# Optimization experiments

Hardware: AMD Instinct MI355X
Metric: run time of the kernel (lower is better)

The kernel has to match this reference:

```python
import jax, jax.numpy as jnp
import numpy as np

N_PROJ, N_SP, D, H = 400000, 40000, 256, 8
DH = D // H  # 32
EPS = 1e-5
NEG_SLOPE = 0.2  # GATv2Conv default


def layer_norm(x, g, b):
    m = x.mean(-1, keepdims=True)
    v = ((x - m) ** 2).mean(-1, keepdims=True)
    return (x - m) / jnp.sqrt(v + EPS) * g + b


def setup_inputs() -> dict:
    key = jax.random.key(0)
    ks = jax.random.split(key, 8)
    w = lambda k, shape: jax.random.normal(k, shape, jnp.float32) * 0.05
    return dict(
        proj_features=jax.random.normal(ks[0], (N_PROJ, D), jnp.float32),
        prev_scenepoint_features=jax.random.normal(ks[1], (N_SP, D), jnp.float32),
        Wl=w(ks[2], (D, D)), bl=jnp.zeros((D,), jnp.float32),
        Wr=w(ks[3], (D, D)), br=jnp.zeros((D,), jnp.float32),
        att=w(ks[4], (H, DH)), gat_bias=jnp.zeros((D,), jnp.float32),
        ln1_g=jnp.ones((D,), jnp.float32), ln1_b=jnp.zeros((D,), jnp.float32),
        ln2_g=jnp.ones((D,), jnp.float32), ln2_b=jnp.zeros((D,), jnp.float32),
        mlp_W=w(ks[5], (D, D)), mlp_b=jnp.zeros((D,), jnp.float32),
        edge_src=jnp.arange(N_PROJ, dtype=jnp.int32),
        edge_tgt=jax.random.randint(ks[6], (N_PROJ,), 0, N_SP, jnp.int32),
    )


def reference(proj_features, prev_scenepoint_features, Wl, bl, Wr, br, att,
              gat_bias, ln1_g, ln1_b, ln2_g, ln2_b, mlp_W, mlp_b,
              edge_src, edge_tgt):
    # norm_and_proj_scenepoint2proj: LayerNorm + ReLU (no Linear: dims equal)
    x_agg = jax.nn.relu(layer_norm(prev_scenepoint_features, ln1_g, ln1_b))

    # GATv2Conv: lin_l on source (projection) nodes, lin_r on target (scene point) nodes
    xl = (proj_features @ Wl + bl).reshape(N_PROJ, H, DH)   # [Np,H,DH]
    xr = (x_agg @ Wr + br).reshape(N_SP, H, DH)             # [Ns,H,DH]
    xl_e = xl[edge_src]                                     # [E,H,DH]
    xr_e = xr[edge_tgt]                                     # [E,H,DH]
    e = jnp.einsum('ehd,hd->eh', jax.nn.leaky_relu(xl_e + xr_e, NEG_SLOPE), att)

    # segment softmax over edges sharing the same target scene point
    e_max = jax.ops.segment_max(e, edge_tgt, num_segments=N_SP)
    ex = jnp.exp(e - e_max[edge_tgt])
    denom = jax.ops.segment_sum(ex, edge_tgt, num_segments=N_SP)
    alpha = ex / (denom[edge_tgt] + 1e-16)                  # [E,H]

    out = jax.ops.segment_sum(alpha[..., None] * xl_e, edge_tgt, num_segments=N_SP)
    x = out.reshape(N_SP, D) + gat_bias                     # concat heads + bias

    # stateful residual with previous scene point features
    x = prev_scenepoint_features + x
    x_skip = x
    # norm_pre_mlp + ReLU, then mlp (single Linear since n_hidden_layers=0)
    x = jax.nn.relu(layer_norm(x, ln2_g, ln2_b))
    x = x @ mlp_W + mlp_b
    return x_skip + x
```

## Files before the change

### kernel.cpp

```cpp
#include <hip/hip_runtime.h>
#include <hip/hip_bf16.h>

#define D_DIM 256
#define EPS_LN 1e-5f
#define NEG_SLOPE 0.2f

typedef __bf16 bf16x8 __attribute__((ext_vector_type(8)));
typedef unsigned short ushortx8 __attribute__((ext_vector_type(8)));
typedef unsigned short ushortx4 __attribute__((ext_vector_type(4)));
typedef float floatx4 __attribute__((ext_vector_type(4)));

__device__ inline unsigned short f2bf(float f) {
    __hip_bfloat16 h = __float2bfloat16(f);
    return __builtin_bit_cast(unsigned short, h);
}
__device__ inline float bf2f(unsigned short u) {
    unsigned int x = ((unsigned int)u) << 16;
    return __builtin_bit_cast(float, x);
}

__global__ __launch_bounds__(256) void wtrans_kernel(
        const float* __restrict__ W0, const float* __restrict__ W1,
        const float* __restrict__ W2, unsigned short* __restrict__ T0,
        unsigned short* __restrict__ T1, unsigned short* __restrict__ T2) {
    const float* W = (blockIdx.y == 0) ? W0 : (blockIdx.y == 1) ? W1 : W2;
    unsigned short* T = (blockIdx.y == 0) ? T0 : (blockIdx.y == 1) ? T1 : T2;
    __shared__ float lds[64][65];
    const int tx = blockIdx.x & 3;
    const int ty = blockIdx.x >> 2;
    const int t = threadIdx.x;
    const int r = t >> 6;
    const int c = t & 63;
#pragma unroll
    for (int i = 0; i < 16; ++i) {
        int row = ty * 64 + r + i * 4;
        lds[r + i * 4][c] = W[row * 256 + tx * 64 + c];
    }
    __syncthreads();
#pragma unroll
    for (int i = 0; i < 16; ++i) {
        int orow = tx * 64 + r + i * 4;
        T[orow * 256 + ty * 64 + c] = f2bf(lds[c][r + i * 4]);
    }
}

__global__ __launch_bounds__(256) void ln_relu_kernel(
        const float* __restrict__ x, const float* __restrict__ g,
        const float* __restrict__ b, float* __restrict__ y, int nrows) {
    int row = blockIdx.x * 4 + (threadIdx.x >> 6);
    if (row >= nrows) return;
    int lane = threadIdx.x & 63;
    float4 v = ((const float4*)(x + (size_t)row * D_DIM))[lane];
    float s = v.x + v.y + v.z + v.w;
    float s2 = v.x * v.x + v.y * v.y + v.z * v.z + v.w * v.w;
#pragma unroll
    for (int m = 32; m >= 1; m >>= 1) {
        s += __shfl_xor(s, m, 64);
        s2 += __shfl_xor(s2, m, 64);
    }
    float mean = s * (1.f / D_DIM);
    float var = s2 * (1.f / D_DIM) - mean * mean;
    float rstd = rsqrtf(var + EPS_LN);
    float4 gv = ((const float4*)g)[lane];
    float4 bv = ((const float4*)b)[lane];
    float4 o;
    o.x = fmaxf((v.x - mean) * rstd * gv.x + bv.x, 0.f);
    o.y = fmaxf((v.y - mean) * rstd * gv.y + bv.y, 0.f);
    o.z = fmaxf((v.z - mean) * rstd * gv.z + bv.z, 0.f);
    o.w = fmaxf((v.w - mean) * rstd * gv.w + bv.w, 0.f);
    ((float4*)(y + (size_t)row * D_DIM))[lane] = o;
}

template <int OUT_BF16, int HAS_RES>
__global__ __launch_bounds__(256) void gemm256_kernel(
        const float* __restrict__ A, const unsigned short* __restrict__ Wt,
        const float* __restrict__ bias, const float* __restrict__ res,
        void* __restrict__ out, int M) {
    __shared__ unsigned short As[2][128 * 40];
    __shared__ unsigned short Bs[2][128 * 40];
    const int n0 = blockIdx.x * 128;
    const int m0 = blockIdx.y * 128;
    const int t = threadIdx.x;
    const int lane = t & 63;
    const int wave = t >> 6;
    const int q = lane >> 4;
    const int l16 = lane & 15;
    const int wm = (wave & 1) * 64;
    const int wn = (wave >> 1) * 64;
    const int sm = t >> 1;
    const int sh = t & 1;

    const bool arow_ok = (m0 + sm) < M;
    const float* aptr = A + (size_t)(m0 + sm) * 256 + sh * 16;
    const unsigned short* bptr = Wt + (size_t)(n0 + sm) * 256 + sh * 16;

    float4 a_reg[4];
    ushortx8 b_reg[2];

    auto g_load = [&](int kt) {
        if (arow_ok) {
            const float4* ap = (const float4*)(aptr + kt * 32);
            a_reg[0] = ap[0]; a_reg[1] = ap[1]; a_reg[2] = ap[2]; a_reg[3] = ap[3];
        }
        const ushortx8* bp = (const ushortx8*)(bptr + kt * 32);
        b_reg[0] = bp[0]; b_reg[1] = bp[1];
    };
    auto s_store = [&](int buf) {
        unsigned short tmp[16];
        if (arow_ok) {
#pragma unroll
            for (int i = 0; i < 4; ++i) {
                tmp[i * 4 + 0] = f2bf(a_reg[i].x);
                tmp[i * 4 + 1] = f2bf(a_reg[i].y);
                tmp[i * 4 + 2] = f2bf(a_reg[i].z);
                tmp[i * 4 + 3] = f2bf(a_reg[i].w);
            }
        } else {
#pragma unroll
            for (int i = 0; i < 16; ++i) tmp[i] = 0;
        }
        *(ushortx8*)&As[buf][sm * 40 + sh * 16] = *(ushortx8*)&tmp[0];
        *(ushortx8*)&As[buf][sm * 40 + sh * 16 + 8] = *(ushortx8*)&tmp[8];
        *(ushortx8*)&Bs[buf][sm * 40 + sh * 16] = b_reg[0];
        *(ushortx8*)&Bs[buf][sm * 40 + sh * 16 + 8] = b_reg[1];
    };

    floatx4 acc[4][4] = {};

    g_load(0);
    s_store(0);
    __syncthreads();

    for (int kt = 0; kt < 8; ++kt) {
        const int cur = kt & 1;
        if (kt < 7) g_load(kt + 1);
        bf16x8 af[4], bfr[4];
#pragma unroll
        for (int mi = 0; mi < 4; ++mi)
            af[mi] = __builtin_bit_cast(bf16x8,
                *(const ushortx8*)&As[cur][(wm + mi * 16 + l16) * 40 + q * 8]);
#pragma unroll
        for (int ni = 0; ni < 4; ++ni)
            bfr[ni] = __builtin_bit_cast(bf16x8,
                *(const ushortx8*)&Bs[cur][(wn + ni * 16 + l16) * 40 + q * 8]);
#pragma unroll
        for (int mi = 0; mi < 4; ++mi)
#pragma unroll
            for (int ni = 0; ni < 4; ++ni)
                acc[mi][ni] = __builtin_amdgcn_mfma_f32_16x16x32_bf16(
                    af[mi], bfr[ni], acc[mi][ni], 0, 0, 0);
        if (kt < 7) {
            s_store(cur ^ 1);
            __syncthreads();
        }
    }

#pragma unroll
    for (int mi = 0; mi < 4; ++mi) {
#pragma unroll
        for (int ni = 0; ni < 4; ++ni) {
            int col = n0 + wn + ni * 16 + l16;
            float bcol = bias[col];
#pragma unroll
            for (int r = 0; r < 4; ++r) {
                int row = m0 + wm + mi * 16 + q * 4 + r;
                if (row < M) {
                    float v = acc[mi][ni][r] + bcol;
                    if (HAS_RES) v += res[(size_t)row * 256 + col];
                    if (OUT_BF16)
                        ((unsigned short*)out)[(size_t)row * 256 + col] = f2bf(v);
                    else
                        ((float*)out)[(size_t)row * 256 + col] = v;
                }
            }
        }
    }
}

__global__ void hist_kernel(const int* __restrict__ tgt, int* __restrict__ counts, int E) {
    int i = blockIdx.x * 256 + threadIdx.x;
    if (i < E) atomicAdd(&counts[tgt[i]], 1);
}

__global__ __launch_bounds__(1024) void scan_kernel(
        const int* __restrict__ counts, int* __restrict__ offs, int n) {
    __shared__ int lds[1024];
    int t = threadIdx.x;
    int CH = (n + 1023) >> 10;
    int beg = t * CH, end = min(beg + CH, n);
    int s = 0;
    for (int i = beg; i < end; ++i) s += counts[i];
    lds[t] = s;
    __syncthreads();
    for (int off = 1; off < 1024; off <<= 1) {
        int v = (t >= off) ? lds[t - off] : 0;
        __syncthreads();
        lds[t] += v;
        __syncthreads();
    }
    int run = lds[t] - s;
    for (int i = beg; i < end; ++i) { offs[i] = run; run += counts[i]; }
    if (t == 1023) offs[n] = lds[1023];
}

__global__ void scatter_kernel(const int* __restrict__ tgt, const int* __restrict__ offs,
                               int* __restrict__ cursor, int* __restrict__ elist, int E) {
    int i = blockIdx.x * 256 + threadIdx.x;
    if (i < E) {
        int tg = tgt[i];
        int p = atomicAdd(&cursor[tg], 1);
        elist[offs[tg] + p] = i;
    }
}

__global__ __launch_bounds__(256) void aggregate_kernel(
        const unsigned short* __restrict__ xl, const float* __restrict__ xr,
        const float* __restrict__ prev, const int* __restrict__ esrc,
        const int* __restrict__ elist, const int* __restrict__ offs,
        const float* __restrict__ att, const float* __restrict__ gbias,
        const float* __restrict__ g2, const float* __restrict__ b2,
        float* __restrict__ x_skip, float* __restrict__ h2, int nsp) {
    int tgt = blockIdx.x * 4 + (threadIdx.x >> 6);
    if (tgt >= nsp) return;
    int lane = threadIdx.x & 63;
    float4 xrv = ((const float4*)(xr + (size_t)tgt * D_DIM))[lane];
    float4 attv = ((const float4*)att)[lane];
    float acc0 = 0.f, acc1 = 0.f, acc2 = 0.f, acc3 = 0.f, den = 0.f;
    int beg = offs[tgt], end = offs[tgt + 1];

    ushortx4 row = {};
    if (beg < end) {
        int e = elist[beg];
        int src = esrc[e];
        row = ((const ushortx4*)(xl + (size_t)src * D_DIM))[lane];
    }
    for (int i = beg; i < end; ++i) {
        ushortx4 row_n = {};
        if (i + 1 < end) {
            int e1 = elist[i + 1];
            int s1 = esrc[e1];
            row_n = ((const ushortx4*)(xl + (size_t)s1 * D_DIM))[lane];
        }
        float x0 = bf2f(row[0]), x1 = bf2f(row[1]), x2 = bf2f(row[2]), x3 = bf2f(row[3]);
        float t0 = x0 + xrv.x, t1 = x1 + xrv.y, t2 = x2 + xrv.z, t3 = x3 + xrv.w;
        t0 = t0 > 0.f ? t0 : NEG_SLOPE * t0;
        t1 = t1 > 0.f ? t1 : NEG_SLOPE * t1;
        t2 = t2 > 0.f ? t2 : NEG_SLOPE * t2;
        t3 = t3 > 0.f ? t3 : NEG_SLOPE * t3;
        float p = t0 * attv.x + t1 * attv.y + t2 * attv.z + t3 * attv.w;
        p += __shfl_xor(p, 1, 64);
        p += __shfl_xor(p, 2, 64);
        p += __shfl_xor(p, 4, 64);
        float ex = __expf(p);
        den += ex;
        acc0 += ex * x0; acc1 += ex * x1; acc2 += ex * x2; acc3 += ex * x3;
        row = row_n;
    }
    float rden = 1.f / (den + 1e-16f);
    float4 pv = ((const float4*)(prev + (size_t)tgt * D_DIM))[lane];
    float4 gb = ((const float4*)gbias)[lane];
    float v0 = pv.x + acc0 * rden + gb.x;
    float v1 = pv.y + acc1 * rden + gb.y;
    float v2 = pv.z + acc2 * rden + gb.z;
    float v3 = pv.w + acc3 * rden + gb.w;
    float s = v0 + v1 + v2 + v3;
    float s2 = v0 * v0 + v1 * v1 + v2 * v2 + v3 * v3;
#pragma unroll
    for (int m = 32; m >= 1; m >>= 1) {
        s += __shfl_xor(s, m, 64);
        s2 += __shfl_xor(s2, m, 64);
    }
    float mean = s * (1.f / D_DIM);
    float var = s2 * (1.f / D_DIM) - mean * mean;
    float rstd = rsqrtf(var + EPS_LN);
    float4 g2v = ((const float4*)g2)[lane];
    float4 b2v = ((const float4*)b2)[lane];
    float4 xs; xs.x = v0; xs.y = v1; xs.z = v2; xs.w = v3;
    ((float4*)(x_skip + (size_t)tgt * D_DIM))[lane] = xs;
    float4 h;
    h.x = fmaxf((v0 - mean) * rstd * g2v.x + b2v.x, 0.f);
    h.y = fmaxf((v1 - mean) * rstd * g2v.y + b2v.y, 0.f);
    h.z = fmaxf((v2 - mean) * rstd * g2v.z + b2v.z, 0.f);
    h.w = fmaxf((v3 - mean) * rstd * g2v.w + b2v.w, 0.f);
    ((float4*)(h2 + (size_t)tgt * D_DIM))[lane] = h;
}

extern "C" void kernel_launch(void* const* d_in, const int* in_sizes, int n_in,
                              void* d_out, int out_size, void* d_ws, size_t ws_size,
                              hipStream_t stream) {
    const float* proj = (const float*)d_in[0];
    const float* prev = (const float*)d_in[1];
    const float* Wl   = (const float*)d_in[2];
    const float* bl   = (const float*)d_in[3];
    const float* Wr   = (const float*)d_in[4];
    const float* br   = (const float*)d_in[5];
    const float* att  = (const float*)d_in[6];
    const float* gbias= (const float*)d_in[7];
    const float* ln1g = (const float*)d_in[8];
    const float* ln1b = (const float*)d_in[9];
    const float* ln2g = (const float*)d_in[10];
    const float* ln2b = (const float*)d_in[11];
    const float* Wm   = (const float*)d_in[12];
    const float* mb   = (const float*)d_in[13];
    const int* esrc   = (const int*)d_in[14];
    const int* etgt   = (const int*)d_in[15];

    const int NP = in_sizes[0] / D_DIM;
    const int NS = in_sizes[1] / D_DIM;
    const int E  = in_sizes[14];

    char* base = (char*)d_ws;
    size_t off = 0;
    auto carve = [&](size_t bytes) {
        char* p = base + off;
        off += (bytes + 255) & ~(size_t)255;
        return p;
    };
    unsigned short* xl    = (unsigned short*)carve((size_t)NP * D_DIM * 2);
    float* x_agg          = (float*)carve((size_t)NS * D_DIM * 4);
    float* xr             = (float*)carve((size_t)NS * D_DIM * 4);
    float* x_skip         = (float*)carve((size_t)NS * D_DIM * 4);
    float* h2             = (float*)carve((size_t)NS * D_DIM * 4);
    unsigned short* Wt_l  = (unsigned short*)carve((size_t)D_DIM * D_DIM * 2);
    unsigned short* Wt_r  = (unsigned short*)carve((size_t)D_DIM * D_DIM * 2);
    unsigned short* Wt_m  = (unsigned short*)carve((size_t)D_DIM * D_DIM * 2);
    int* counts           = (int*)carve((size_t)NS * 4 * 2);
    int* cursor           = counts + NS;
    int* offs             = (int*)carve((size_t)(NS + 1) * 4);
    int* elist            = (int*)carve((size_t)E * 4);

    hipMemsetAsync(counts, 0, (size_t)NS * 4 * 2, stream);

    wtrans_kernel<<<dim3(16, 3), 256, 0, stream>>>(Wl, Wr, Wm, Wt_l, Wt_r, Wt_m);

    ln_relu_kernel<<<(NS + 3) / 4, 256, 0, stream>>>(prev, ln1g, ln1b, x_agg, NS);

    gemm256_kernel<0, 0><<<dim3(2, (NS + 127) / 128), 256, 0, stream>>>(
        x_agg, Wt_r, br, nullptr, (void*)xr, NS);

    gemm256_kernel<1, 0><<<dim3(2, (NP + 127) / 128), 256, 0, stream>>>(
        proj, Wt_l, bl, nullptr, (void*)xl, NP);

    hist_kernel<<<(E + 255) / 256, 256, 0, stream>>>(etgt, counts, E);
    scan_kernel<<<1, 1024, 0, stream>>>(counts, offs, NS);
    scatter_kernel<<<(E + 255) / 256, 256, 0, stream>>>(etgt, offs, cursor, elist, E);

    aggregate_kernel<<<(NS + 3) / 4, 256, 0, stream>>>(
        xl, xr, prev, esrc, elist, offs, att, gbias, ln2g, ln2b, x_skip, h2, NS);

    gemm256_kernel<0, 1><<<dim3(2, (NS + 127) / 128), 256, 0, stream>>>(
        h2, Wt_m, mb, x_skip, d_out, NS);
}
```

Baseline: 1.048 ms.

## Stage GEMM tiles via async global-to-LDS copies and store source ids in edge list

The GEMM now loads fp32 A tiles and bf16 weight tiles straight from global memory into LDS with global_load_lds, using XOR-swizzled layouts. The fp32-to-bf16 conversion moves to fragment-read time, and launch bounds request 3 blocks per SM. This drops the register staging round-trip and overlaps the next tile's loads with MFMA work, but it doubles A's LDS footprint and repeats the conversion for each wave. Separately, the scatter kernel writes source ids directly, so the aggregate kernel skips one dependent indirection per edge.

```diff
diff --git a/kernel.cpp b/kernel.cpp
--- a/kernel.cpp
+++ b/kernel.cpp
@@ -17,6 +17,19 @@
 __device__ inline float bf2f(unsigned short u) {
     unsigned int x = ((unsigned int)u) << 16;
     return __builtin_bit_cast(float, x);
+}
+
+__device__ __forceinline__ void async_copy16(const void* g, void* l) {
+    __builtin_amdgcn_global_load_lds(
+        (const __attribute__((address_space(1))) unsigned int*)g,
+        (__attribute__((address_space(3))) unsigned int*)l, 16, 0, 0);
+}
+
+__device__ inline bf16x8 cvt_frag(float4 a, float4 b) {
+    ushortx8 u;
+    u[0] = f2bf(a.x); u[1] = f2bf(a.y); u[2] = f2bf(a.z); u[3] = f2bf(a.w);
+    u[4] = f2bf(b.x); u[5] = f2bf(b.y); u[6] = f2bf(b.z); u[7] = f2bf(b.w);
+    return __builtin_bit_cast(bf16x8, u);
 }
 
 __global__ __launch_bounds__(256) void wtrans_kernel(
@@ -72,12 +85,12 @@
 }
 
 template <int OUT_BF16, int HAS_RES>
-__global__ __launch_bounds__(256) void gemm256_kernel(
+__global__ __launch_bounds__(256, 3) void gemm256_kernel(
         const float* __restrict__ A, const unsigned short* __restrict__ Wt,
         const float* __restrict__ bias, const float* __restrict__ res,
         void* __restrict__ out, int M) {
-    __shared__ unsigned short As[2][128 * 40];
-    __shared__ unsigned short Bs[2][128 * 40];
+    __shared__ float As[2][128 * 32];
+    __shared__ unsigned short Bs[2][128 * 32];
     const int n0 = blockIdx.x * 128;
     const int m0 = blockIdx.y * 128;
     const int t = threadIdx.x;
@@ -87,72 +100,61 @@
     const int l16 = lane & 15;
     const int wm = (wave & 1) * 64;
     const int wn = (wave >> 1) * 64;
-    const int sm = t >> 1;
-    const int sh = t & 1;
-
-    const bool arow_ok = (m0 + sm) < M;
-    const float* aptr = A + (size_t)(m0 + sm) * 256 + sh * 16;
-    const unsigned short* bptr = Wt + (size_t)(n0 + sm) * 256 + sh * 16;
-
-    float4 a_reg[4];
-    ushortx8 b_reg[2];
-
-    auto g_load = [&](int kt) {
-        if (arow_ok) {
-            const float4* ap = (const float4*)(aptr + kt * 32);
-            a_reg[0] = ap[0]; a_reg[1] = ap[1]; a_reg[2] = ap[2]; a_reg[3] = ap[3];
-        }
-        const ushortx8* bp = (const ushortx8*)(bptr + kt * 32);
-        b_reg[0] = bp[0]; b_reg[1] = bp[1];
+
+    const int rowLA = lane >> 3;
+    const int GA = (lane & 7) ^ (rowLA & 7);
+    const int rowLB = lane >> 2;
+    const int GB = (lane & 3) ^ ((lane >> 3) & 3);
+
+    auto stage = [&](int buf, int kt) {
+#pragma unroll
+        for (int i = 0; i < 4; ++i) {
+            int s = wave * 4 + i;
+            int row = m0 + s * 8 + rowLA;
+            row = row < M ? row : (M - 1);
+            async_copy16(A + (size_t)row * 256 + kt * 32 + GA * 4,
+                         &As[buf][s * 256]);
+        }
+#pragma unroll
+        for (int i = 0; i < 2; ++i) {
+            int s = wave * 2 + i;
+            int row = n0 + s * 16 + rowLB;
+            async_copy16(Wt + (size_t)row * 256 + kt * 32 + GB * 8,
+                         &Bs[buf][s * 512]);
+        }
     };
-    auto s_store = [&](int buf) {
-        unsigned short tmp[16];
-        if (arow_ok) {
-#pragma unroll
-            for (int i = 0; i < 4; ++i) {
-                tmp[i * 4 + 0] = f2bf(a_reg[i].x);
-                tmp[i * 4 + 1] = f2bf(a_reg[i].y);
-                tmp[i * 4 + 2] = f2bf(a_reg[i].z);
-                tmp[i * 4 + 3] = f2bf(a_reg[i].w);
-            }
-        } else {
-#pragma unroll
-            for (int i = 0; i < 16; ++i) tmp[i] = 0;
-        }
-        *(ushortx8*)&As[buf][sm * 40 + sh * 16] = *(ushortx8*)&tmp[0];
-        *(ushortx8*)&As[buf][sm * 40 + sh * 16 + 8] = *(ushortx8*)&tmp[8];
-        *(ushortx8*)&Bs[buf][sm * 40 + sh * 16] = b_reg[0];
-        *(ushortx8*)&Bs[buf][sm * 40 + sh * 16 + 8] = b_reg[1];
-    };
 
     floatx4 acc[4][4] = {};
 
-    g_load(0);
-    s_store(0);
+    stage(0, 0);
     __syncthreads();
 
     for (int kt = 0; kt < 8; ++kt) {
         const int cur = kt & 1;
-        if (kt < 7) g_load(kt + 1);
+        if (kt < 7) stage(cur ^ 1, kt + 1);
         bf16x8 af[4], bfr[4];
 #pragma unroll
-        for (int mi = 0; mi < 4; ++mi)
-            af[mi] = __builtin_bit_cast(bf16x8,
-                *(const ushortx8*)&As[cur][(wm + mi * 16 + l16) * 40 + q * 8]);
-#pragma unroll
-        for (int ni = 0; ni < 4; ++ni)
+        for (int mi = 0; mi < 4; ++mi) {
+            int r = wm + mi * 16 + l16;
+            int P0 = (2 * q) ^ (r & 7);
+            float4 f0 = *(const float4*)&As[cur][r * 32 + P0 * 4];
+            float4 f1 = *(const float4*)&As[cur][r * 32 + (P0 ^ 1) * 4];
+            af[mi] = cvt_frag(f0, f1);
+        }
+#pragma unroll
+        for (int ni = 0; ni < 4; ++ni) {
+            int r = wn + ni * 16 + l16;
+            int P = q ^ ((r >> 1) & 3);
             bfr[ni] = __builtin_bit_cast(bf16x8,
-                *(const ushortx8*)&Bs[cur][(wn + ni * 16 + l16) * 40 + q * 8]);
+                *(const ushortx8*)&Bs[cur][r * 32 + P * 8]);
+        }
 #pragma unroll
         for (int mi = 0; mi < 4; ++mi)
 #pragma unroll
             for (int ni = 0; ni < 4; ++ni)
                 acc[mi][ni] = __builtin_amdgcn_mfma_f32_16x16x32_bf16(
                     af[mi], bfr[ni], acc[mi][ni], 0, 0, 0);
-        if (kt < 7) {
-            s_store(cur ^ 1);
-            __syncthreads();
-        }
+        __syncthreads();
     }
 
 #pragma unroll
@@ -203,23 +205,24 @@
     if (t == 1023) offs[n] = lds[1023];
 }
 
-__global__ void scatter_kernel(const int* __restrict__ tgt, const int* __restrict__ offs,
-                               int* __restrict__ cursor, int* __restrict__ elist, int E) {
+__global__ void scatter_kernel(const int* __restrict__ tgt, const int* __restrict__ src,
+                               const int* __restrict__ offs, int* __restrict__ cursor,
+                               int* __restrict__ slist, int E) {
     int i = blockIdx.x * 256 + threadIdx.x;
     if (i < E) {
         int tg = tgt[i];
         int p = atomicAdd(&cursor[tg], 1);
-        elist[offs[tg] + p] = i;
+        slist[offs[tg] + p] = src[i];
     }
 }
 
 __global__ __launch_bounds__(256) void aggregate_kernel(
         const unsigned short* __restrict__ xl, const float* __restrict__ xr,
-        const float* __restrict__ prev, const int* __restrict__ esrc,
-        const int* __restrict__ elist, const int* __restrict__ offs,
-        const float* __restrict__ att, const float* __restrict__ gbias,
-        const float* __restrict__ g2, const float* __restrict__ b2,
-        float* __restrict__ x_skip, float* __restrict__ h2, int nsp) {
+        const float* __restrict__ prev, const int* __restrict__ slist,
+        const int* __restrict__ offs, const float* __restrict__ att,
+        const float* __restrict__ gbias, const float* __restrict__ g2,
+        const float* __restrict__ b2, float* __restrict__ x_skip,
+        float* __restrict__ h2, int nsp) {
     int tgt = blockIdx.x * 4 + (threadIdx.x >> 6);
     if (tgt >= nsp) return;
     int lane = threadIdx.x & 63;
@@ -230,15 +233,13 @@
 
     ushortx4 row = {};
     if (beg < end) {
-        int e = elist[beg];
-        int src = esrc[e];
+        int src = slist[beg];
         row = ((const ushortx4*)(xl + (size_t)src * D_DIM))[lane];
     }
     for (int i = beg; i < end; ++i) {
         ushortx4 row_n = {};
         if (i + 1 < end) {
-            int e1 = elist[i + 1];
-            int s1 = esrc[e1];
+            int s1 = slist[i + 1];
             row_n = ((const ushortx4*)(xl + (size_t)s1 * D_DIM))[lane];
         }
         float x0 = bf2f(row[0]), x1 = bf2f(row[1]), x2 = bf2f(row[2]), x3 = bf2f(row[3]);
@@ -327,7 +328,7 @@
     int* counts           = (int*)carve((size_t)NS * 4 * 2);
     int* cursor           = counts + NS;
     int* offs             = (int*)carve((size_t)(NS + 1) * 4);
-    int* elist            = (int*)carve((size_t)E * 4);
+    int* slist            = (int*)carve((size_t)E * 4);
 
     hipMemsetAsync(counts, 0, (size_t)NS * 4 * 2, stream);
 
@@ -343,10 +344,10 @@
 
     hist_kernel<<<(E + 255) / 256, 256, 0, stream>>>(etgt, counts, E);
     scan_kernel<<<1, 1024, 0, stream>>>(counts, offs, NS);
-    scatter_kernel<<<(E + 255) / 256, 256, 0, stream>>>(etgt, offs, cursor, elist, E);
+    scatter_kernel<<<(E + 255) / 256, 256, 0, stream>>>(etgt, esrc, offs, cursor, slist, E);
 
     aggregate_kernel<<<(NS + 3) / 4, 256, 0, stream>>>(
-        xl, xr, prev, esrc, elist, offs, att, gbias, ln2g, ln2b, x_skip, h2, NS);
+        xl, xr, prev, slist, offs, att, gbias, ln2g, ln2b, x_skip, h2, NS);
 
     gemm256_kernel<0, 1><<<dim3(2, (NS + 127) / 128), 256, 0, stream>>>(
         h2, Wt_m, mb, x_skip, d_out, NS);
```

Result: faster. 970.0 us (-7.4%).
